# Kernel tuning notes

Measured on AMD Instinct MI355X. Metric: run time of the kernel, lower is better.

Reference implementation:

```python
import jax, jax.numpy as jnp
import numpy as np

B, N, H, DH, ORDER, DEG = 64, 256, 8, 64, 4, 16
D = H * DH
TOTAL = B * N
E = TOTAL * DEG


def setup_inputs() -> dict:
    key = jax.random.key(0)
    ks = jax.random.split(key, 16)
    output = jax.random.normal(ks[0], (N, B, D), dtype=jnp.float32)
    # attention weights: positive, row-normalized like softmax output
    attn = jax.nn.softmax(jax.random.normal(ks[1], (B, H, N, N), dtype=jnp.float32), axis=-1)
    out_each_head = jax.random.normal(ks[2], (B, N, H, DH), dtype=jnp.float32)
    # random graph edges, endpoints within the same graph (global node ids)
    g = jax.random.randint(ks[3], (E,), 0, B)
    s = g * N + jax.random.randint(ks[4], (E,), 0, N)
    d = g * N + jax.random.randint(ks[5], (E,), 0, N)
    edge_index = jnp.stack([s, d], axis=0).astype(jnp.int64)
    # full graphs, no padding: feature_indices[:,0]=graph id, [:,1]=node pos
    fi = jnp.stack([jnp.repeat(jnp.arange(B), N), jnp.tile(jnp.arange(N), B)], axis=1).astype(jnp.int64)
    batch = fi[:, 0]
    sc = 0.1
    params = dict(
        W_gcn=jax.random.normal(ks[6], (ORDER, ORDER)) * sc,
        b_gcn=jnp.zeros((ORDER,), jnp.float32),
        W_lin=jax.random.normal(ks[7], (ORDER, ORDER)) * sc,
        b_lin=jnp.zeros((ORDER,), jnp.float32),
        W_cheb=jax.random.normal(ks[8], (ORDER, DH, DH)) * sc,
        b_cheb=jnp.zeros((DH,), jnp.float32),
        W_cat=jax.random.normal(ks[9], (2 * D, D)) * sc,
        b_cat=jnp.zeros((D,), jnp.float32),
        gamma=jnp.ones((D,), jnp.float32),
        beta=jnp.zeros((D,), jnp.float32),
    )
    return dict(output=output, attn=attn, out_each_head=out_each_head,
                edge_index=edge_index, feature_indices=fi, batch=batch, **params)


def reference(output, attn, out_each_head, edge_index, feature_indices, batch,
              W_gcn, b_gcn, W_lin, b_lin, W_cheb, b_cheb, W_cat, b_cat, gamma, beta):
    Bn, Hn, Nn, _ = attn.shape
    C = W_gcn.shape[0]
    total = Bn * Nn
    NT = Hn * total

    # ---- get_filter_coefficients: GCN over fully-connected attention graphs ----
    # edge weights are detached in the original (edge_weight.detach())
    A = jax.lax.stop_gradient(attn).transpose(1, 0, 2, 3).reshape(Hn * Bn, Nn, Nn)
    A_hat = A + jnp.eye(Nn, dtype=A.dtype)  # add self loops (weight 1)
    deg = A_hat.sum(axis=1)                 # deg_j = sum_i A_hat[i,j]
    dinv = jnp.where(deg > 0, jax.lax.rsqrt(deg), 0.0)  # (HB, N)
    # x = ones, so x @ W_gcn is a constant row = column sums of W_gcn
    w_row = W_gcn.sum(axis=0)               # (C,)
    s = jnp.einsum('bi,bij->bj', dinv, A_hat) * dinv     # (HB, N)
    x_c = jnp.tanh(s[:, :, None] * w_row + b_gcn)        # (HB, N, C)
    gap = x_c.mean(axis=1)                  # global avg pool per graph (HB, C)
    coeff = gap @ W_lin + b_lin             # (HB, C) rows ordered (head, batch)

    # ---- dynamic Chebyshev filtering per head on the input graph ----
    offsets = (jnp.arange(Hn) * total).astype(edge_index.dtype)
    src = (edge_index[0][None, :] + offsets[:, None]).reshape(-1)
    dst = (edge_index[1][None, :] + offsets[:, None]).reshape(-1)
    deg_n = jax.ops.segment_sum(jnp.ones(src.shape[0], jnp.float32), dst, num_segments=NT)
    dinv_n = jnp.where(deg_n > 0, jax.lax.rsqrt(deg_n), 0.0)
    norm_e = -(dinv_n[src] * dinv_n[dst])   # scaled Laplacian L_hat = -D^-1/2 A D^-1/2

    def prop(x):  # L_hat @ x via gather/scatter
        return jax.ops.segment_sum(norm_e[:, None] * x[src], dst, num_segments=NT)

    # nodes ordered (head, batch, node)
    x0 = out_each_head.transpose(2, 0, 1, 3).reshape(NT, DH)
    batch_all = (batch[None, :] + (jnp.arange(Hn) * Bn)[:, None]).reshape(-1)  # graph id h*B+b
    c_node = coeff[batch_all]               # (NT, ORDER) per-node dynamic coefficients

    T_prev, T_cur = x0, prop(x0)
    acc = c_node[:, 0:1] * (T_prev @ W_cheb[0]) + c_node[:, 1:2] * (T_cur @ W_cheb[1])
    for k in range(2, C):
        T_next = 2.0 * prop(T_cur) - T_prev
        acc = acc + c_node[:, k:k + 1] * (T_next @ W_cheb[k])
        T_prev, T_cur = T_cur, T_next
    acc = acc + b_cheb                      # (NT, DH)

    # regroup heads: (H, B*N, DH) -> (B*N, H*DH), scatter back to (N, B, D)
    filtered = acc.reshape(Hn, total, DH).transpose(1, 0, 2).reshape(total, Hn * DH)
    out_filtered = jnp.zeros_like(output).at[feature_indices[:, 1], feature_indices[:, 0], :].set(filtered)

    # skip connection + linear_cat + final LayerNorm
    out_cat = jnp.concatenate([output, out_filtered], axis=-1)
    out = out_cat @ W_cat + b_cat
    mu = out.mean(axis=-1, keepdims=True)
    var = ((out - mu) ** 2).mean(axis=-1, keepdims=True)
    out = (out - mu) * jax.lax.rsqrt(var + 1e-5) * gamma + beta
    return out
```

## Files before the change

kernel.cpp:

```cpp
#include <hip/hip_runtime.h>
#include <stdint.h>

#define Bq      64
#define Nq      256
#define Hq      8
#define DHq     64
#define TOTALq  16384
#define NTq     131072
#define Dq      512

typedef __attribute__((ext_vector_type(8))) short short8;
typedef __attribute__((ext_vector_type(4))) float floatx4;

__device__ __forceinline__ unsigned short f2bf(float f) {
    union { float f; unsigned int u; } c; c.f = f;
    unsigned int u = c.u;
    return (unsigned short)((u + 0x7fffu + ((u >> 16) & 1u)) >> 16);
}
__device__ __forceinline__ float bf2f(unsigned short u) {
    union { unsigned int u; float f; } c; c.u = ((unsigned int)u) << 16;
    return c.f;
}


__global__ void count_deg_kernel(const int* __restrict__ dstp, int* __restrict__ cnt, int E) {
    int e = blockIdx.x * 256 + threadIdx.x;
    if (e < E) atomicAdd(&cnt[dstp[e]], 1);
}

__global__ void dinv_kernel(const int* __restrict__ cnt, float* __restrict__ dinv_n) {
    int v = blockIdx.x * 256 + threadIdx.x;
    if (v < TOTALq) {
        int c = cnt[v];
        dinv_n[v] = (c > 0) ? rsqrtf((float)c) : 0.0f;
    }
}

__global__ void pscatter_kernel(const int* __restrict__ srcp, const int* __restrict__ dstp,
                                const float* __restrict__ dinv_n, float* __restrict__ Pf, int E) {
    int e = blockIdx.x * 256 + threadIdx.x;
    if (e >= E) return;
    int s = srcp[e], d = dstp[e];
    int g = d >> 8;
    atomicAdd(&Pf[((size_t)g << 16) + ((size_t)(d & 255) << 8) + (s & 255)],
              -(dinv_n[s] * dinv_n[d]));
}

__global__ void pconv_kernel(const float* __restrict__ Pf, unsigned short* __restrict__ Pb) {
    int i = (blockIdx.x * 256 + threadIdx.x) * 4;
    float4 v = *(const float4*)(Pf + i);
    unsigned int lo = (unsigned int)f2bf(v.x) | ((unsigned int)f2bf(v.y) << 16);
    unsigned int hi = (unsigned int)f2bf(v.z) | ((unsigned int)f2bf(v.w) << 16);
    *(uint2*)(Pb + i) = make_uint2(lo, hi);
}

__global__ void x0t_kernel(const float* __restrict__ X, unsigned short* __restrict__ Xt) {
    __shared__ float tile[64 * 68];
    int t = threadIdx.x;
    int n0 = blockIdx.x * 64, c0 = blockIdx.y * 64;
#pragma unroll
    for (int it = 0; it < 4; ++it) {
        int idx = it * 256 + t;
        int nr = idx >> 4, sub = idx & 15;
        float4 v = *(const float4*)(X + (size_t)(n0 + nr) * 512 + c0 + sub * 4);
        *(float4*)(&tile[nr * 68 + sub * 4]) = v;
    }
    __syncthreads();
#pragma unroll
    for (int it = 0; it < 2; ++it) {
        int idx = it * 256 + t;
        int cr = idx >> 3, sub = idx & 7;
        unsigned int pk[4];
#pragma unroll
        for (int q = 0; q < 4; ++q) {
            unsigned short a = f2bf(tile[(sub * 8 + q * 2 + 0) * 68 + cr]);
            unsigned short b = f2bf(tile[(sub * 8 + q * 2 + 1) * 68 + cr]);
            pk[q] = (unsigned int)a | ((unsigned int)b << 16);
        }
        *(uint4*)(Xt + (size_t)(c0 + cr) * 16384 + n0 + sub * 8) =
            make_uint4(pk[0], pk[1], pk[2], pk[3]);
    }
}

__global__ void trn_kernel(const unsigned short* __restrict__ Tt, unsigned short* __restrict__ Tn) {
    __shared__ unsigned short tile[64 * 72];
    int t = threadIdx.x;
    int n0 = blockIdx.x * 64, c0 = blockIdx.y * 64;
#pragma unroll
    for (int it = 0; it < 2; ++it) {
        int idx = it * 256 + t;
        int cr = idx >> 3, sub = idx & 7;
        uint4 v = *(const uint4*)(Tt + (size_t)(c0 + cr) * 16384 + n0 + sub * 8);
        *(uint4*)(&tile[cr * 72 + sub * 8]) = v;
    }
    __syncthreads();
#pragma unroll
    for (int it = 0; it < 2; ++it) {
        int idx = it * 256 + t;
        int nr = idx >> 3, sub = idx & 7;
        unsigned int pk[4];
#pragma unroll
        for (int q = 0; q < 4; ++q) {
            unsigned short a = tile[(sub * 8 + q * 2 + 0) * 72 + nr];
            unsigned short b = tile[(sub * 8 + q * 2 + 1) * 72 + nr];
            pk[q] = (unsigned int)a | ((unsigned int)b << 16);
        }
        *(uint4*)(Tn + (size_t)(n0 + nr) * 512 + c0 + sub * 8) =
            make_uint4(pk[0], pk[1], pk[2], pk[3]);
    }
}

__global__ void wchebt_kernel(const float* __restrict__ W, unsigned short* __restrict__ WT) {
    int idx = blockIdx.x * 256 + threadIdx.x;
    int k = idx >> 12, rem = idx & 4095;
    int n = rem >> 6, j = rem & 63;
    WT[idx] = f2bf(W[(k << 12) + (j << 6) + n]);
}

__global__ void coeff_kernel(const float* __restrict__ attn,
                             const float* __restrict__ Wg, const float* __restrict__ bg,
                             const float* __restrict__ Wlin, const float* __restrict__ blin,
                             float* __restrict__ coeff) {
    __shared__ float dinv[Nq];
    __shared__ float red[16];
    int g = blockIdx.x;
    int h = g >> 6;
    int b = g & 63;
    const float* A = attn + ((size_t)(b * Hq + h)) * (Nq * Nq);
    int j = threadIdx.x;

    float cs = 0.0f;
    for (int i = 0; i < Nq; ++i) cs += A[i * Nq + j];
    float dv = rsqrtf(cs + 1.0f);
    dinv[j] = dv;
    __syncthreads();

    float sj = dv;
    for (int i = 0; i < Nq; ++i) sj += dinv[i] * A[i * Nq + j];
    sj *= dv;

    float xc[4];
#pragma unroll
    for (int c = 0; c < 4; ++c) {
        float wr = Wg[0 * 4 + c] + Wg[1 * 4 + c] + Wg[2 * 4 + c] + Wg[3 * 4 + c];
        xc[c] = tanhf(sj * wr + bg[c]);
    }
    int lane = j & 63, wv = j >> 6;
#pragma unroll
    for (int c = 0; c < 4; ++c) {
        float v = xc[c];
#pragma unroll
        for (int o = 32; o >= 1; o >>= 1) v += __shfl_down(v, o, 64);
        if (lane == 0) red[wv * 4 + c] = v;
    }
    __syncthreads();
    if (j < 4) {
        float gap[4];
#pragma unroll
        for (int c = 0; c < 4; ++c)
            gap[c] = (red[0 + c] + red[4 + c] + red[8 + c] + red[12 + c]) * (1.0f / 256.0f);
        float v = blin[j];
#pragma unroll
        for (int c = 0; c < 4; ++c) v += gap[c] * Wlin[c * 4 + j];
        coeff[g * 4 + j] = v;
    }
}

__global__ __launch_bounds__(256, 2)
void cheb_prop(const unsigned short* __restrict__ Pb,
               const unsigned short* __restrict__ Tc,
               const unsigned short* __restrict__ Tp,
               unsigned short* __restrict__ Tn, int first) {
    __shared__ unsigned short A_lds[128 * 40];
    __shared__ unsigned short B_lds[128 * 40];
    const int b = blockIdx.x, mb = blockIdx.y, cb = blockIdx.z;
    const int tid = threadIdx.x, lane = tid & 63, wv = tid >> 6;
    const int wr = wv & 1, wc = wv >> 1, quad = lane >> 4, l15 = lane & 15;
    const unsigned short* Pbase = Pb + ((size_t)b << 16) + (size_t)mb * 128 * 256;

    floatx4 acc[4][4];
#pragma unroll
    for (int rt = 0; rt < 4; ++rt)
#pragma unroll
        for (int ct = 0; ct < 4; ++ct) acc[rt][ct] = (floatx4){0.f, 0.f, 0.f, 0.f};

    for (int kt = 0; kt < 8; ++kt) {
        const int kc = kt * 32;
        __syncthreads();
#pragma unroll
        for (int it = 0; it < 2; ++it) {
            int idx = it * 256 + tid;
            int row = idx >> 2, sub = idx & 3;
            *(uint4*)(A_lds + row * 40 + sub * 8) =
                *(const uint4*)(Pbase + row * 256 + kc + sub * 8);
            *(uint4*)(B_lds + row * 40 + sub * 8) =
                *(const uint4*)(Tc + (size_t)(cb * 128 + row) * 16384 + b * 256 + kc + sub * 8);
        }
        __syncthreads();
        short8 af[4], bfr[4];
#pragma unroll
        for (int rt = 0; rt < 4; ++rt)
            af[rt] = *(const short8*)(A_lds + (wr * 64 + rt * 16 + l15) * 40 + quad * 8);
#pragma unroll
        for (int ct = 0; ct < 4; ++ct)
            bfr[ct] = *(const short8*)(B_lds + (wc * 64 + ct * 16 + l15) * 40 + quad * 8);
#pragma unroll
        for (int rt = 0; rt < 4; ++rt)
#pragma unroll
            for (int ct = 0; ct < 4; ++ct)
                acc[rt][ct] = __builtin_amdgcn_mfma_f32_16x16x32_bf16(af[rt], bfr[ct],
                                                                     acc[rt][ct], 0, 0, 0);
    }
#pragma unroll
    for (int rt = 0; rt < 4; ++rt)
#pragma unroll
        for (int ct = 0; ct < 4; ++ct) {
            int col = cb * 128 + wc * 64 + ct * 16 + l15;
            int m = mb * 128 + wr * 64 + rt * 16 + quad * 4;
            size_t base = (size_t)col * 16384 + b * 256 + m;
            float v[4];
            if (first) {
#pragma unroll
                for (int i = 0; i < 4; ++i) v[i] = acc[rt][ct][i];
            } else {
                uint2 tp = *(const uint2*)(Tp + base);
                v[0] = 2.0f * acc[rt][ct][0] - bf2f((unsigned short)(tp.x & 0xffff));
                v[1] = 2.0f * acc[rt][ct][1] - bf2f((unsigned short)(tp.x >> 16));
                v[2] = 2.0f * acc[rt][ct][2] - bf2f((unsigned short)(tp.y & 0xffff));
                v[3] = 2.0f * acc[rt][ct][3] - bf2f((unsigned short)(tp.y >> 16));
            }
            unsigned int lo = (unsigned int)f2bf(v[0]) | ((unsigned int)f2bf(v[1]) << 16);
            unsigned int hi = (unsigned int)f2bf(v[2]) | ((unsigned int)f2bf(v[3]) << 16);
            *(uint2*)(Tn + base) = make_uint2(lo, hi);
        }
}

__global__ __launch_bounds__(256, 2)
void filt_kernel(const float* __restrict__ oeh,
                 const unsigned short* __restrict__ T1n, const unsigned short* __restrict__ T2n,
                 const unsigned short* __restrict__ T3n, const unsigned short* __restrict__ WchT,
                 const float* __restrict__ coeff, const float* __restrict__ bch,
                 unsigned short* __restrict__ filtb) {
    __shared__ unsigned short A_lds[256 * 72];
    __shared__ unsigned short W_lds[64 * 72];
    const int b = blockIdx.x, h = blockIdx.y;
    const int tid = threadIdx.x, lane = tid & 63, wv = tid >> 6;
    const int quad = lane >> 4, l15 = lane & 15;

    floatx4 acc[4][4];
#pragma unroll
    for (int rt = 0; rt < 4; ++rt)
#pragma unroll
        for (int ct = 0; ct < 4; ++ct) acc[rt][ct] = (floatx4){0.f, 0.f, 0.f, 0.f};

    for (int k = 0; k < 4; ++k) {
        float ck = coeff[(h * Bq + b) * 4 + k];
        __syncthreads();
        if (k == 0) {
#pragma unroll
            for (int it = 0; it < 8; ++it) {
                int idx = it * 256 + tid;
                int row = idx >> 3, sub = idx & 7;
                const float* sp = oeh + (size_t)(b * 256 + row) * 512 + h * 64 + sub * 8;
                float4 v0 = *(const float4*)sp;
                float4 v1 = *(const float4*)(sp + 4);
                unsigned int p0 = (unsigned int)f2bf(v0.x * ck) | ((unsigned int)f2bf(v0.y * ck) << 16);
                unsigned int p1 = (unsigned int)f2bf(v0.z * ck) | ((unsigned int)f2bf(v0.w * ck) << 16);
                unsigned int p2 = (unsigned int)f2bf(v1.x * ck) | ((unsigned int)f2bf(v1.y * ck) << 16);
                unsigned int p3 = (unsigned int)f2bf(v1.z * ck) | ((unsigned int)f2bf(v1.w * ck) << 16);
                *(uint4*)(A_lds + row * 72 + sub * 8) = make_uint4(p0, p1, p2, p3);
            }
        } else {
            const unsigned short* Tk = (k == 1) ? T1n : (k == 2) ? T2n : T3n;
#pragma unroll
            for (int it = 0; it < 8; ++it) {
                int idx = it * 256 + tid;
                int row = idx >> 3, sub = idx & 7;
                uint4 tv = *(const uint4*)(Tk + (size_t)(b * 256 + row) * 512 + h * 64 + sub * 8);
                unsigned int w[4] = {tv.x, tv.y, tv.z, tv.w};
                unsigned int o[4];
#pragma unroll
                for (int q = 0; q < 4; ++q) {
                    float lo = bf2f((unsigned short)(w[q] & 0xffff)) * ck;
                    float hi = bf2f((unsigned short)(w[q] >> 16)) * ck;
                    o[q] = (unsigned int)f2bf(lo) | ((unsigned int)f2bf(hi) << 16);
                }
                *(uint4*)(A_lds + row * 72 + sub * 8) = make_uint4(o[0], o[1], o[2], o[3]);
            }
        }
#pragma unroll
        for (int it = 0; it < 2; ++it) {
            int idx = it * 256 + tid;
            int r = idx >> 3, sub = idx & 7;
            *(uint4*)(W_lds + r * 72 + sub * 8) =
                *(const uint4*)(WchT + k * 4096 + r * 64 + sub * 8);
        }
        __syncthreads();
#pragma unroll
        for (int kk = 0; kk < 2; ++kk) {
            short8 af[4], bfr[4];
#pragma unroll
            for (int rt = 0; rt < 4; ++rt)
                af[rt] = *(const short8*)(A_lds + (wv * 64 + rt * 16 + l15) * 72 + kk * 32 + quad * 8);
#pragma unroll
            for (int ct = 0; ct < 4; ++ct)
                bfr[ct] = *(const short8*)(W_lds + (ct * 16 + l15) * 72 + kk * 32 + quad * 8);
#pragma unroll
            for (int rt = 0; rt < 4; ++rt)
#pragma unroll
                for (int ct = 0; ct < 4; ++ct)
                    acc[rt][ct] = __builtin_amdgcn_mfma_f32_16x16x32_bf16(af[rt], bfr[ct],
                                                                         acc[rt][ct], 0, 0, 0);
        }
    }
#pragma unroll
    for (int rt = 0; rt < 4; ++rt)
#pragma unroll
        for (int ct = 0; ct < 4; ++ct) {
            int coln = ct * 16 + l15;
            float bias = bch[coln];
#pragma unroll
            for (int i = 0; i < 4; ++i) {
                int m = wv * 64 + rt * 16 + quad * 4 + i;
                size_t r = (size_t)m * 64 + b;
                filtb[r * 512 + h * 64 + coln] = f2bf(acc[rt][ct][i] + bias);
            }
        }
}

__global__ void wt2_kernel(const float* __restrict__ W, unsigned short* __restrict__ Wt2) {
    int idx = blockIdx.x * 256 + threadIdx.x;
    int col = idx & 511;
    int ktq = idx >> 9;
    const float* src = W + (size_t)(ktq * 8) * 512 + col;
    unsigned int pk[4];
#pragma unroll
    for (int q2 = 0; q2 < 4; ++q2) {
        unsigned short a = f2bf(src[(q2 * 2 + 0) * 512]);
        unsigned short b = f2bf(src[(q2 * 2 + 1) * 512]);
        pk[q2] = (unsigned int)a | ((unsigned int)b << 16);
    }
    *(uint4*)(Wt2 + (size_t)idx * 8) = make_uint4(pk[0], pk[1], pk[2], pk[3]);
}

__global__ __launch_bounds__(512, 2)
void gemm_ln_mfma(const float* __restrict__ outp, const unsigned short* __restrict__ filtb,
                  const unsigned short* __restrict__ Wt2, const float* __restrict__ bcat,
                  const float* __restrict__ gamma, const float* __restrict__ beta,
                  float* __restrict__ out) {
    extern __shared__ unsigned char smc[];
    unsigned short* A_lds0 = (unsigned short*)smc;
    unsigned short* A_lds1 = (unsigned short*)(smc + 4096);
    float* ep = (float*)smc;

    const int tid = threadIdx.x;
    const int lane = tid & 63;
    const int wv = tid >> 6;
    const int quad = lane >> 4;
    const int l15 = lane & 15;
    const int r0 = blockIdx.x * 64;

    const int s_row = tid >> 3;
    const int s_sub = tid & 7;
    const int s_q   = s_sub >> 1;
    const int s_e   = (s_sub & 1) * 4;

    const size_t boff = (size_t)(quad * 512 + wv * 64 + l15) * 8;

    floatx4 acc[4][4];
#pragma unroll
    for (int rt = 0; rt < 4; ++rt)
#pragma unroll
        for (int ct = 0; ct < 4; ++ct) acc[rt][ct] = (floatx4){0.f, 0.f, 0.f, 0.f};

    short8 bA[4], bB[4];

    {
#pragma unroll
        for (int ct = 0; ct < 4; ++ct)
            bA[ct] = *(const short8*)(Wt2 + boff + ct * 128);
        float4 av = *(const float4*)(outp + (size_t)(r0 + s_row) * 512 + s_sub * 4);
        uint2 ap;
        ap.x = (unsigned int)f2bf(av.x) | ((unsigned int)f2bf(av.y) << 16);
        ap.y = (unsigned int)f2bf(av.z) | ((unsigned int)f2bf(av.w) << 16);
        *(uint2*)(A_lds0 + (s_q * 64 + s_row) * 8 + s_e) = ap;
        __syncthreads();
    }

#define GSTEP(KT, BC, BN, AC, AN, HASNEXT)                                          \
    do {                                                                            \
        const int kt_ = (KT);                                                       \
        const bool hn_ = (HASNEXT);                                                 \
        const bool isf_ = (kt_ + 1 < 16);                                           \
        float4 av_; uint2 afb_;                                                     \
        if (hn_) {                                                                  \
            _Pragma("unroll")                                                       \
            for (int ct = 0; ct < 4; ++ct)                                          \
                BN[ct] = *(const short8*)(Wt2 + (size_t)(kt_ + 1) * 16384 +         \
                                          boff + ct * 128);                         \
            const int kc_ = (kt_ + 1) * 32;                                         \
            if (isf_)                                                               \
                av_ = *(const float4*)(outp + (size_t)(r0 + s_row) * 512 +          \
                                       kc_ + s_sub * 4);                            \
            else                                                                    \
                afb_ = *(const uint2*)(filtb + (size_t)(r0 + s_row) * 512 +         \
                                       (kc_ - 512) + s_sub * 4);                    \
        }                                                                           \
        short8 af_[4];                                                              \
        _Pragma("unroll")                                                           \
        for (int rt = 0; rt < 4; ++rt)                                              \
            af_[rt] = *(const short8*)(AC + (quad * 64 + rt * 16 + l15) * 8);       \
        _Pragma("unroll")                                                           \
        for (int rt = 0; rt < 4; ++rt)                                              \
            _Pragma("unroll")                                                       \
            for (int ct = 0; ct < 4; ++ct)                                          \
                acc[rt][ct] = __builtin_amdgcn_mfma_f32_16x16x32_bf16(              \
                    af_[rt], BC[ct], acc[rt][ct], 0, 0, 0);                         \
        if (hn_) {                                                                  \
            uint2 ap_;                                                              \
            if (isf_) {                                                             \
                ap_.x = (unsigned int)f2bf(av_.x) | ((unsigned int)f2bf(av_.y) << 16); \
                ap_.y = (unsigned int)f2bf(av_.z) | ((unsigned int)f2bf(av_.w) << 16); \
            } else {                                                                \
                ap_ = afb_;                                                         \
            }                                                                       \
            *(uint2*)(AN + (s_q * 64 + s_row) * 8 + s_e) = ap_;                     \
        }                                                                           \
        __syncthreads();                                                            \
    } while (0)

    for (int kt2 = 0; kt2 < 16; ++kt2) {
        GSTEP(2 * kt2,     bA, bB, A_lds0, A_lds1, true);
        GSTEP(2 * kt2 + 1, bB, bA, A_lds1, A_lds0, kt2 < 15);
    }
#undef GSTEP

    float gg[8], bb[8];
#pragma unroll
    for (int i = 0; i < 8; ++i) { gg[i] = gamma[i * 64 + lane]; bb[i] = beta[i * 64 + lane]; }
    float bc[4];
#pragma unroll
    for (int ct = 0; ct < 4; ++ct) bc[ct] = bcat[wv * 64 + ct * 16 + l15];

    for (int half = 0; half < 2; ++half) {
        __syncthreads();
#pragma unroll
        for (int rt2 = 0; rt2 < 2; ++rt2) {
            const int rt = half * 2 + rt2;
#pragma unroll
            for (int ct = 0; ct < 4; ++ct) {
                const int col = wv * 64 + ct * 16 + l15;
#pragma unroll
                for (int i = 0; i < 4; ++i) {
                    const int row_l = rt2 * 16 + quad * 4 + i;
                    ep[row_l * 512 + col] = acc[rt][ct][i] + bc[ct];
                }
            }
        }
        __syncthreads();
#pragma unroll
        for (int m4 = 0; m4 < 4; ++m4) {
            const int m = wv * 4 + m4;
            float s = 0.0f, ss = 0.0f;
#pragma unroll
            for (int i = 0; i < 8; ++i) {
                float v = ep[m * 512 + i * 64 + lane];
                s += v; ss += v * v;
            }
#pragma unroll
            for (int o = 32; o >= 1; o >>= 1) {
                s += __shfl_down(s, o, 64);
                ss += __shfl_down(ss, o, 64);
            }
            s = __shfl(s, 0, 64);
            ss = __shfl(ss, 0, 64);
            const float mu = s * (1.0f / 512.0f);
            const float var = ss * (1.0f / 512.0f) - mu * mu;
            const float rs = rsqrtf(var + 1e-5f);
            const int r = r0 + half * 32 + m;
#pragma unroll
            for (int i = 0; i < 8; ++i) {
                const int d = i * 64 + lane;
                out[(size_t)r * 512 + d] = (ep[m * 512 + d] - mu) * rs * gg[i] + bb[i];
            }
        }
    }
}

extern "C" void kernel_launch(void* const* d_in, const int* in_sizes, int n_in,
                              void* d_out, int out_size, void* d_ws, size_t ws_size,
                              hipStream_t stream) {
    const float* output       = (const float*)d_in[0];
    const float* attn         = (const float*)d_in[1];
    const float* oeh          = (const float*)d_in[2];
    const int*   edge_index   = (const int*)d_in[3];
    const float* W_gcn        = (const float*)d_in[6];
    const float* b_gcn        = (const float*)d_in[7];
    const float* W_lin        = (const float*)d_in[8];
    const float* b_lin        = (const float*)d_in[9];
    const float* W_cheb       = (const float*)d_in[10];
    const float* b_cheb       = (const float*)d_in[11];
    const float* W_cat        = (const float*)d_in[12];
    const float* b_cat        = (const float*)d_in[13];
    const float* gamma        = (const float*)d_in[14];
    const float* beta         = (const float*)d_in[15];
    float* out = (float*)d_out;

    const int E = in_sizes[3] / 2;
    const int* srcp = edge_index;
    const int* dstp = edge_index + E;

    uint8_t* ws = (uint8_t*)d_ws;
    size_t cur = 0;
    auto alloc = [&](size_t bytes) -> void* {
        void* p = ws + cur;
        cur += (bytes + 255) & ~(size_t)255;
        return p;
    };
    int*   cnt     = (int*)alloc(TOTALq * sizeof(int));
    float* dinv_n  = (float*)alloc(TOTALq * sizeof(float));
    float* Pf      = (float*)alloc((size_t)64 * 65536 * sizeof(float));
    unsigned short* Pb   = (unsigned short*)alloc((size_t)64 * 65536 * 2);
    float* coeff   = (float*)alloc(512 * 4 * sizeof(float));
    unsigned short* X0_t = (unsigned short*)alloc((size_t)512 * 16384 * 2);
    unsigned short* T1_t = (unsigned short*)alloc((size_t)512 * 16384 * 2);
    unsigned short* T2_t = (unsigned short*)alloc((size_t)512 * 16384 * 2);
    unsigned short* T3_t = (unsigned short*)alloc((size_t)512 * 16384 * 2);
    unsigned short* WchT = (unsigned short*)alloc(4 * 64 * 64 * 2);
    unsigned short* Wt2  = (unsigned short*)alloc((size_t)Dq * 1024 * 2);
    unsigned short* filtb = (unsigned short*)alloc((size_t)TOTALq * Dq * sizeof(float));
    unsigned short* T1_n = (unsigned short*)Pf;
    unsigned short* T2_n = X0_t;
    unsigned short* T3_n = T1_t;
    (void)ws_size; (void)n_in; (void)out_size;

    hipMemsetAsync(cnt, 0, TOTALq * sizeof(int), stream);
    count_deg_kernel<<<(E + 255) / 256, 256, 0, stream>>>(dstp, cnt, E);
    dinv_kernel<<<TOTALq / 256, 256, 0, stream>>>(cnt, dinv_n);
    hipMemsetAsync(Pf, 0, (size_t)64 * 65536 * sizeof(float), stream);
    pscatter_kernel<<<(E + 255) / 256, 256, 0, stream>>>(srcp, dstp, dinv_n, Pf, E);
    pconv_kernel<<<4096, 256, 0, stream>>>(Pf, Pb);

    x0t_kernel<<<dim3(256, 8), 256, 0, stream>>>(oeh, X0_t);
    coeff_kernel<<<Hq * Bq, 256, 0, stream>>>(attn, W_gcn, b_gcn, W_lin, b_lin, coeff);
    wt2_kernel<<<256, 256, 0, stream>>>(W_cat, Wt2);
    wchebt_kernel<<<64, 256, 0, stream>>>(W_cheb, WchT);

    dim3 pg(64, 2, 4);
    cheb_prop<<<pg, 256, 0, stream>>>(Pb, X0_t, nullptr, T1_t, 1);
    cheb_prop<<<pg, 256, 0, stream>>>(Pb, T1_t, X0_t, T2_t, 0);
    cheb_prop<<<pg, 256, 0, stream>>>(Pb, T2_t, T1_t, T3_t, 0);

    trn_kernel<<<dim3(256, 8), 256, 0, stream>>>(T1_t, T1_n);
    trn_kernel<<<dim3(256, 8), 256, 0, stream>>>(T2_t, T2_n);
    trn_kernel<<<dim3(256, 8), 256, 0, stream>>>(T3_t, T3_n);

    filt_kernel<<<dim3(64, 8), 256, 0, stream>>>(oeh, T1_n, T2_n, T3_n, WchT, coeff,
                                                 b_cheb, filtb);

    gemm_ln_mfma<<<TOTALq / 64, 512, 65536, stream>>>(output, filtb, Wt2, b_cat,
                                                      gamma, beta, out);
}
```

Baseline: 465.0 us.

## Fuse Chebyshev transposes into filter kernel and vectorize coefficient reduction

Removes the three separate transpose kernels by having the filter kernel read the channel-major T buffers directly and transpose them into swizzled LDS. The per-graph coefficient scale moves from the activations onto the Chebyshev weights, which are now kept in fp32 and scaled and converted per block. The coefficient kernel is rewritten to use 512 threads with float4 row loads and LDS partial sums instead of column-strided scalar loops. This saves several full passes over the T buffers and speeds the attention reduction, at the cost of scalar strided LDS writes in the filter kernel and a slight change in rounding order.

```diff
diff --git a/kernel.cpp b/kernel.cpp
--- a/kernel.cpp
+++ b/kernel.cpp
@@ -82,87 +82,86 @@
     }
 }
 
-__global__ void trn_kernel(const unsigned short* __restrict__ Tt, unsigned short* __restrict__ Tn) {
-    __shared__ unsigned short tile[64 * 72];
-    int t = threadIdx.x;
-    int n0 = blockIdx.x * 64, c0 = blockIdx.y * 64;
-#pragma unroll
-    for (int it = 0; it < 2; ++it) {
-        int idx = it * 256 + t;
-        int cr = idx >> 3, sub = idx & 7;
-        uint4 v = *(const uint4*)(Tt + (size_t)(c0 + cr) * 16384 + n0 + sub * 8);
-        *(uint4*)(&tile[cr * 72 + sub * 8]) = v;
-    }
-    __syncthreads();
-#pragma unroll
-    for (int it = 0; it < 2; ++it) {
-        int idx = it * 256 + t;
-        int nr = idx >> 3, sub = idx & 7;
-        unsigned int pk[4];
-#pragma unroll
-        for (int q = 0; q < 4; ++q) {
-            unsigned short a = tile[(sub * 8 + q * 2 + 0) * 72 + nr];
-            unsigned short b = tile[(sub * 8 + q * 2 + 1) * 72 + nr];
-            pk[q] = (unsigned int)a | ((unsigned int)b << 16);
-        }
-        *(uint4*)(Tn + (size_t)(n0 + nr) * 512 + c0 + sub * 8) =
-            make_uint4(pk[0], pk[1], pk[2], pk[3]);
-    }
-}
-
-__global__ void wchebt_kernel(const float* __restrict__ W, unsigned short* __restrict__ WT) {
+__global__ void wchebt_kernel(const float* __restrict__ W, float* __restrict__ WT) {
     int idx = blockIdx.x * 256 + threadIdx.x;
     int k = idx >> 12, rem = idx & 4095;
     int n = rem >> 6, j = rem & 63;
-    WT[idx] = f2bf(W[(k << 12) + (j << 6) + n]);
-}
-
-__global__ void coeff_kernel(const float* __restrict__ attn,
-                             const float* __restrict__ Wg, const float* __restrict__ bg,
-                             const float* __restrict__ Wlin, const float* __restrict__ blin,
-                             float* __restrict__ coeff) {
-    __shared__ float dinv[Nq];
-    __shared__ float red[16];
-    int g = blockIdx.x;
-    int h = g >> 6;
-    int b = g & 63;
+    WT[idx] = W[(k << 12) + (j << 6) + n];
+}
+
+__global__ __launch_bounds__(512)
+void coeff_kernel(const float* __restrict__ attn,
+                  const float* __restrict__ Wg, const float* __restrict__ bg,
+                  const float* __restrict__ Wlin, const float* __restrict__ blin,
+                  float* __restrict__ coeff) {
+    __shared__ floatx4 part[8][64];
+    __shared__ floatx4 dinv4[64];
+    const int g = blockIdx.x;
+    const int h = g >> 6;
+    const int b = g & 63;
     const float* A = attn + ((size_t)(b * Hq + h)) * (Nq * Nq);
-    int j = threadIdx.x;
-
-    float cs = 0.0f;
-    for (int i = 0; i < Nq; ++i) cs += A[i * Nq + j];
-    float dv = rsqrtf(cs + 1.0f);
-    dinv[j] = dv;
+    const int tid = threadIdx.x;
+    const int rg = tid >> 6;
+    const int cv = tid & 63;
+    const float* Ap = A + cv * 4;
+
+    floatx4 s1 = (floatx4){0.f, 0.f, 0.f, 0.f};
+#pragma unroll 8
+    for (int r = 0; r < 32; ++r)
+        s1 += *(const floatx4*)(Ap + (size_t)(rg * 32 + r) * 256);
+    part[rg][cv] = s1;
     __syncthreads();
 
-    float sj = dv;
-    for (int i = 0; i < Nq; ++i) sj += dinv[i] * A[i * Nq + j];
-    sj *= dv;
-
-    float xc[4];
-#pragma unroll
-    for (int c = 0; c < 4; ++c) {
-        float wr = Wg[0 * 4 + c] + Wg[1 * 4 + c] + Wg[2 * 4 + c] + Wg[3 * 4 + c];
-        xc[c] = tanhf(sj * wr + bg[c]);
-    }
-    int lane = j & 63, wv = j >> 6;
-#pragma unroll
-    for (int c = 0; c < 4; ++c) {
-        float v = xc[c];
-#pragma unroll
-        for (int o = 32; o >= 1; o >>= 1) v += __shfl_down(v, o, 64);
-        if (lane == 0) red[wv * 4 + c] = v;
+    if (tid < 64) {
+        floatx4 cs = part[0][tid];
+#pragma unroll
+        for (int i = 1; i < 8; ++i) cs += part[i][tid];
+        floatx4 dv;
+#pragma unroll
+        for (int i = 0; i < 4; ++i) dv[i] = rsqrtf(cs[i] + 1.0f);
+        dinv4[tid] = dv;
     }
     __syncthreads();
-    if (j < 4) {
-        float gap[4];
-#pragma unroll
-        for (int c = 0; c < 4; ++c)
-            gap[c] = (red[0 + c] + red[4 + c] + red[8 + c] + red[12 + c]) * (1.0f / 256.0f);
-        float v = blin[j];
-#pragma unroll
-        for (int c = 0; c < 4; ++c) v += gap[c] * Wlin[c * 4 + j];
-        coeff[g * 4 + j] = v;
+
+    const float* dsc = (const float*)dinv4;
+    floatx4 s2 = (floatx4){0.f, 0.f, 0.f, 0.f};
+#pragma unroll 8
+    for (int r = 0; r < 32; ++r) {
+        int rr = rg * 32 + r;
+        s2 += dsc[rr] * (*(const floatx4*)(Ap + (size_t)rr * 256));
+    }
+    part[rg][cv] = s2;
+    __syncthreads();
+
+    if (tid < 64) {
+        floatx4 ws = part[0][tid];
+#pragma unroll
+        for (int i = 1; i < 8; ++i) ws += part[i][tid];
+        floatx4 dv = dinv4[tid];
+        floatx4 sj = (ws + dv) * dv;
+
+        float wr[4], bgl[4];
+#pragma unroll
+        for (int c = 0; c < 4; ++c) {
+            wr[c]  = Wg[0 * 4 + c] + Wg[1 * 4 + c] + Wg[2 * 4 + c] + Wg[3 * 4 + c];
+            bgl[c] = bg[c];
+        }
+        float v[4];
+#pragma unroll
+        for (int c = 0; c < 4; ++c) {
+            v[c] = tanhf(sj[0] * wr[c] + bgl[c]) + tanhf(sj[1] * wr[c] + bgl[c]) +
+                   tanhf(sj[2] * wr[c] + bgl[c]) + tanhf(sj[3] * wr[c] + bgl[c]);
+#pragma unroll
+            for (int o = 32; o >= 1; o >>= 1) v[c] += __shfl_down(v[c], o, 64);
+        }
+        float g0 = __shfl(v[0], 0, 64), g1 = __shfl(v[1], 0, 64);
+        float g2 = __shfl(v[2], 0, 64), g3 = __shfl(v[3], 0, 64);
+        if (tid < 4) {
+            float r = blin[tid] + (g0 * Wlin[0 * 4 + tid] + g1 * Wlin[1 * 4 + tid] +
+                                   g2 * Wlin[2 * 4 + tid] + g3 * Wlin[3 * 4 + tid]) *
+                                      (1.0f / 256.0f);
+            coeff[g * 4 + tid] = r;
+        }
     }
 }
 
@@ -237,8 +236,8 @@
 
 __global__ __launch_bounds__(256, 2)
 void filt_kernel(const float* __restrict__ oeh,
-                 const unsigned short* __restrict__ T1n, const unsigned short* __restrict__ T2n,
-                 const unsigned short* __restrict__ T3n, const unsigned short* __restrict__ WchT,
+                 const unsigned short* __restrict__ T1t, const unsigned short* __restrict__ T2t,
+                 const unsigned short* __restrict__ T3t, const float* __restrict__ WchTf,
                  const float* __restrict__ coeff, const float* __restrict__ bch,
                  unsigned short* __restrict__ filtb) {
     __shared__ unsigned short A_lds[256 * 72];
@@ -264,44 +263,61 @@
                 const float* sp = oeh + (size_t)(b * 256 + row) * 512 + h * 64 + sub * 8;
                 float4 v0 = *(const float4*)sp;
                 float4 v1 = *(const float4*)(sp + 4);
-                unsigned int p0 = (unsigned int)f2bf(v0.x * ck) | ((unsigned int)f2bf(v0.y * ck) << 16);
-                unsigned int p1 = (unsigned int)f2bf(v0.z * ck) | ((unsigned int)f2bf(v0.w * ck) << 16);
-                unsigned int p2 = (unsigned int)f2bf(v1.x * ck) | ((unsigned int)f2bf(v1.y * ck) << 16);
-                unsigned int p3 = (unsigned int)f2bf(v1.z * ck) | ((unsigned int)f2bf(v1.w * ck) << 16);
-                *(uint4*)(A_lds + row * 72 + sub * 8) = make_uint4(p0, p1, p2, p3);
+                unsigned int p0 = (unsigned int)f2bf(v0.x) | ((unsigned int)f2bf(v0.y) << 16);
+                unsigned int p1 = (unsigned int)f2bf(v0.z) | ((unsigned int)f2bf(v0.w) << 16);
+                unsigned int p2 = (unsigned int)f2bf(v1.x) | ((unsigned int)f2bf(v1.y) << 16);
+                unsigned int p3 = (unsigned int)f2bf(v1.z) | ((unsigned int)f2bf(v1.w) << 16);
+                *(uint4*)(A_lds + row * 72 + ((sub ^ ((row >> 3) & 7)) << 3)) =
+                    make_uint4(p0, p1, p2, p3);
             }
         } else {
-            const unsigned short* Tk = (k == 1) ? T1n : (k == 2) ? T2n : T3n;
-#pragma unroll
-            for (int it = 0; it < 8; ++it) {
+            const unsigned short* Tk = (k == 1) ? T1t : (k == 2) ? T2t : T3t;
+            const unsigned short* base = Tk + (size_t)(h * 64) * 16384 + b * 256;
+#pragma unroll
+            for (int it = 0; it < 4; ++it) {
                 int idx = it * 256 + tid;
-                int row = idx >> 3, sub = idx & 7;
-                uint4 tv = *(const uint4*)(Tk + (size_t)(b * 256 + row) * 512 + h * 64 + sub * 8);
-                unsigned int w[4] = {tv.x, tv.y, tv.z, tv.w};
-                unsigned int o[4];
-#pragma unroll
-                for (int q = 0; q < 4; ++q) {
-                    float lo = bf2f((unsigned short)(w[q] & 0xffff)) * ck;
-                    float hi = bf2f((unsigned short)(w[q] >> 16)) * ck;
-                    o[q] = (unsigned int)f2bf(lo) | ((unsigned int)f2bf(hi) << 16);
+                int cr2 = idx >> 5;
+                int nch = idx & 31;
+                int n0 = nch * 8;
+                int crA = cr2 * 2;
+                uint4 a  = *(const uint4*)(base + (size_t)crA * 16384 + n0);
+                uint4 c4 = *(const uint4*)(base + (size_t)(crA + 1) * 16384 + n0);
+                unsigned swz = (unsigned)((((crA >> 3) ^ (nch & 7)) << 3) + (crA & 7));
+                unsigned short* dst = A_lds + swz;
+                unsigned av[4] = {a.x, a.y, a.z, a.w};
+                unsigned cv4[4] = {c4.x, c4.y, c4.z, c4.w};
+#pragma unroll
+                for (int w2 = 0; w2 < 4; ++w2) {
+                    unsigned lo = (av[w2] & 0xffffu) | (cv4[w2] << 16);
+                    unsigned hi = (av[w2] >> 16) | (cv4[w2] & 0xffff0000u);
+                    *(unsigned*)(dst + (n0 + w2 * 2 + 0) * 72) = lo;
+                    *(unsigned*)(dst + (n0 + w2 * 2 + 1) * 72) = hi;
                 }
-                *(uint4*)(A_lds + row * 72 + sub * 8) = make_uint4(o[0], o[1], o[2], o[3]);
             }
         }
 #pragma unroll
         for (int it = 0; it < 2; ++it) {
             int idx = it * 256 + tid;
             int r = idx >> 3, sub = idx & 7;
-            *(uint4*)(W_lds + r * 72 + sub * 8) =
-                *(const uint4*)(WchT + k * 4096 + r * 64 + sub * 8);
+            const float* wp = WchTf + k * 4096 + r * 64 + sub * 8;
+            float4 w0 = *(const float4*)wp;
+            float4 w1 = *(const float4*)(wp + 4);
+            unsigned int p0 = (unsigned int)f2bf(w0.x * ck) | ((unsigned int)f2bf(w0.y * ck) << 16);
+            unsigned int p1 = (unsigned int)f2bf(w0.z * ck) | ((unsigned int)f2bf(w0.w * ck) << 16);
+            unsigned int p2 = (unsigned int)f2bf(w1.x * ck) | ((unsigned int)f2bf(w1.y * ck) << 16);
+            unsigned int p3 = (unsigned int)f2bf(w1.z * ck) | ((unsigned int)f2bf(w1.w * ck) << 16);
+            *(uint4*)(W_lds + r * 72 + sub * 8) = make_uint4(p0, p1, p2, p3);
         }
         __syncthreads();
 #pragma unroll
         for (int kk = 0; kk < 2; ++kk) {
             short8 af[4], bfr[4];
 #pragma unroll
-            for (int rt = 0; rt < 4; ++rt)
-                af[rt] = *(const short8*)(A_lds + (wv * 64 + rt * 16 + l15) * 72 + kk * 32 + quad * 8);
+            for (int rt = 0; rt < 4; ++rt) {
+                int node = wv * 64 + rt * 16 + l15;
+                int blk = ((kk << 2) + quad) ^ ((node >> 3) & 7);
+                af[rt] = *(const short8*)(A_lds + node * 72 + (blk << 3));
+            }
 #pragma unroll
             for (int ct = 0; ct < 4; ++ct)
                 bfr[ct] = *(const short8*)(W_lds + (ct * 16 + l15) * 72 + kk * 32 + quad * 8);
@@ -526,12 +542,9 @@
     unsigned short* T1_t = (unsigned short*)alloc((size_t)512 * 16384 * 2);
     unsigned short* T2_t = (unsigned short*)alloc((size_t)512 * 16384 * 2);
     unsigned short* T3_t = (unsigned short*)alloc((size_t)512 * 16384 * 2);
-    unsigned short* WchT = (unsigned short*)alloc(4 * 64 * 64 * 2);
+    float* WchTf   = (float*)alloc(4 * 64 * 64 * sizeof(float));
     unsigned short* Wt2  = (unsigned short*)alloc((size_t)Dq * 1024 * 2);
-    unsigned short* filtb = (unsigned short*)alloc((size_t)TOTALq * Dq * sizeof(float));
-    unsigned short* T1_n = (unsigned short*)Pf;
-    unsigned short* T2_n = X0_t;
-    unsigned short* T3_n = T1_t;
+    unsigned short* filtb = (unsigned short*)alloc((size_t)TOTALq * Dq * 2);
     (void)ws_size; (void)n_in; (void)out_size;
 
     hipMemsetAsync(cnt, 0, TOTALq * sizeof(int), stream);
@@ -542,20 +555,16 @@
     pconv_kernel<<<4096, 256, 0, stream>>>(Pf, Pb);
 
     x0t_kernel<<<dim3(256, 8), 256, 0, stream>>>(oeh, X0_t);
-    coeff_kernel<<<Hq * Bq, 256, 0, stream>>>(attn, W_gcn, b_gcn, W_lin, b_lin, coeff);
+    coeff_kernel<<<Hq * Bq, 512, 0, stream>>>(attn, W_gcn, b_gcn, W_lin, b_lin, coeff);
     wt2_kernel<<<256, 256, 0, stream>>>(W_cat, Wt2);
-    wchebt_kernel<<<64, 256, 0, stream>>>(W_cheb, WchT);
+    wchebt_kernel<<<64, 256, 0, stream>>>(W_cheb, WchTf);
 
     dim3 pg(64, 2, 4);
     cheb_prop<<<pg, 256, 0, stream>>>(Pb, X0_t, nullptr, T1_t, 1);
     cheb_prop<<<pg, 256, 0, stream>>>(Pb, T1_t, X0_t, T2_t, 0);
     cheb_prop<<<pg, 256, 0, stream>>>(Pb, T2_t, T1_t, T3_t, 0);
 
-    trn_kernel<<<dim3(256, 8), 256, 0, stream>>>(T1_t, T1_n);
-    trn_kernel<<<dim3(256, 8), 256, 0, stream>>>(T2_t, T2_n);
-    trn_kernel<<<dim3(256, 8), 256, 0, stream>>>(T3_t, T3_n);
-
-    filt_kernel<<<dim3(64, 8), 256, 0, stream>>>(oeh, T1_n, T2_n, T3_n, WchT, coeff,
+    filt_kernel<<<dim3(64, 8), 256, 0, stream>>>(oeh, T1_t, T2_t, T3_t, WchTf, coeff,
                                                  b_cheb, filtb);
 
     gemm_ln_mfma<<<TOTALq / 64, 512, 65536, stream>>>(output, filtb, Wt2, b_cat,
```

After: 437.0 us. 1.06x faster.
